# Performance work log

Measured on AMD Instinct MI355X. Metric: run time of the kernel, lower is better.

Reference implementation:

```python
import jax, jax.numpy as jnp
import numpy as np

D = 40       # d_model
SL = 10      # sequenceLength
AN = 268     # actionNum
B = 8192     # batch


def relu6(x):
    return jnp.clip(x, 0.0, 6.0)


def setup_inputs() -> dict:
    key = jax.random.key(0)
    ks = jax.random.split(key, 16)
    s = 1.0 / np.sqrt(D)
    X = jax.random.randint(ks[0], (B, SL, 4), 0, AN)
    t1 = jax.random.randint(ks[1], (B, SL - 1), 0, 7)
    t2 = jax.random.randint(ks[2], (B, SL - 1), 0, 8)
    # per-step Linear(1, D): weight [D,1] -> store as [SL-1, D]; kaiming-uniform bound 1/sqrt(1)=1
    Ew = jax.random.uniform(ks[3], (SL - 1, D), minval=-1.0, maxval=1.0)
    Eb = jax.random.uniform(ks[4], (SL - 1, D), minval=-1.0, maxval=1.0)
    Qw = jax.random.uniform(ks[5], (SL - 1, D, D), minval=-s, maxval=s)
    Qb = jax.random.uniform(ks[6], (SL - 1, D), minval=-s, maxval=s)
    Lw = jax.random.uniform(ks[7], (SL - 1, D * D, D), minval=-s, maxval=s)
    Lb = jax.random.uniform(ks[8], (SL - 1, D * D), minval=-s, maxval=s)
    Mw = jax.random.uniform(ks[9], (SL - 1, D, D), minval=-s, maxval=s)
    Mb = jax.random.uniform(ks[10], (SL - 1, D), minval=-s, maxval=s)
    Tw = jax.random.uniform(ks[11], (AN, D), minval=-s, maxval=s)
    Tb = jax.random.uniform(ks[12], (AN,), minval=-s, maxval=s)
    emb = jax.random.normal(ks[13], (AN, D))
    return dict(X=X, t1=t1, t2=t2, Ew=Ew, Eb=Eb, Qw=Qw, Qb=Qb, Lw=Lw, Lb=Lb,
                Mw=Mw, Mb=Mb, Tw=Tw, Tb=Tb, emb=emb)


def reference(X, t1, t2, Ew, Eb, Qw, Qb, Lw, Lb, Mw, Mb, Tw, Tb, emb):
    b = X.shape[0]
    t = (t1 * 8 + t2).astype(jnp.float32)          # [B, SL-1]
    ae = emb[X[:, :SL - 1, 3]]                     # [B, SL-1, D]

    def step(carry, xs):
        h0, p0 = carry
        ew, eb, qw, qb, lw, lb, mw, mb, ti, ei = xs
        # E(t_i) + Q(p0), both [B, D]
        p1 = relu6(ti[:, None] * ew[None, :] + eb + p0 @ qw.T + qb)
        # hypernetwork-generated per-sample matrix [B, D, D]
        jt = relu6(p1 @ lw.T + lb).reshape(b, D, D)
        tt = jnp.einsum('bd,bde->be', h0, jt)
        h1 = relu6(ei @ mw.T + mb + tt)
        return (h1, p1), None

    xs = (Ew, Eb, Qw, Qb, Lw, Lb, Mw, Mb, t.T, jnp.swapaxes(ae, 0, 1))
    init = (jnp.zeros((b, D), jnp.float32), jnp.zeros((b, D), jnp.float32))
    (h0, _), _ = jax.lax.scan(step, init, xs)
    return h0 @ Tw.T + Tb                          # [B, AN]
```

## Files before the change

### kernel.cpp

```cpp
#include <hip/hip_runtime.h>

#define DD 40
#define SLM1 9
#define ANUM 268
#define MB 32

typedef __attribute__((ext_vector_type(8))) short short8;
typedef __attribute__((ext_vector_type(4))) float f32x4;
typedef __attribute__((ext_vector_type(16))) float f32x16;

#define WS_LW ((size_t)0)
#define WS_QW ((size_t)1105920)
#define WS_MW ((size_t)1133568)
#define WS_TW ((size_t)1161216)

__device__ __forceinline__ unsigned short f2bf(float f){
  unsigned int u = __float_as_uint(f);
  u += 0x7FFFu + ((u >> 16) & 1u);
  return (unsigned short)(u >> 16);
}
__device__ __forceinline__ float relu6f(float v){
  return fminf(fmaxf(v, 0.0f), 6.0f);
}

__device__ __forceinline__ f32x16 mfma3(short8 a0, short8 a1, short8 a2,
                                        short8 b0, short8 b1, short8 b2){
  f32x16 c = {0,0,0,0,0,0,0,0,0,0,0,0,0,0,0,0};
  c = __builtin_amdgcn_mfma_f32_32x32x16_bf16(a0, b0, c, 0, 0, 0);
  c = __builtin_amdgcn_mfma_f32_32x32x16_bf16(a1, b1, c, 0, 0, 0);
  c = __builtin_amdgcn_mfma_f32_32x32x16_bf16(a2, b2, c, 0, 0, 0);
  return c;
}

__global__ __launch_bounds__(256)
void prep_frags(const float* __restrict__ Qw, const float* __restrict__ Lw,
                const float* __restrict__ Mw, const float* __restrict__ Tw,
                const float* __restrict__ Ew, const float* __restrict__ Eb,
                const float* __restrict__ Qb, const float* __restrict__ Lb,
                const float* __restrict__ Mb, const float* __restrict__ Tb,
                unsigned short* __restrict__ ws)
{
  const int bid = blockIdx.x, tid = threadIdx.x;
  if (bid < 360){
    int s = bid / 40, d = bid - s*40;
    unsigned short* dst = ws + WS_LW + (size_t)bid*3072;
    const float* W = Lw + (size_t)s*64000;
    const float* bv = Lb + (size_t)s*1600;
    for (int i = tid; i < 3072; i += 256){
      int et = i / 1536, r = i - et*1536;
      int kf = r >> 9, q = r & 511, l = q >> 3, j = q & 7;
      int k = kf*16 + ((l >> 5) << 3) + j;
      int e = et*32 + (l & 31);
      float v = 0.f;
      if (e < DD){
        int n = d*DD + e;
        if (k < DD) v = W[n*DD + k];
        else if (k == DD) v = bv[n];
      }
      dst[i] = f2bf(v);
    }
  } else if (bid < 369){
    int s = bid - 360;
    unsigned short* dst = ws + WS_QW + (size_t)s*3072;
    const float* W = Qw + (size_t)s*1600;
    for (int i = tid; i < 3072; i += 256){
      int et = i / 1536, r = i - et*1536;
      int kf = r >> 9, q = r & 511, l = q >> 3, j = q & 7;
      int k = kf*16 + ((l >> 5) << 3) + j;
      int jc = et*32 + (l & 31);
      float v = 0.f;
      if (jc < DD){
        if (k < DD) v = W[jc*DD + k];
        else if (k == DD) v = Eb[s*DD + jc] + Qb[s*DD + jc];
        else if (k == DD+1) v = Ew[s*DD + jc];
      }
      dst[i] = f2bf(v);
    }
  } else if (bid < 378){
    int s = bid - 369;
    unsigned short* dst = ws + WS_MW + (size_t)s*3072;
    const float* W = Mw + (size_t)s*1600;
    for (int i = tid; i < 3072; i += 256){
      int et = i / 1536, r = i - et*1536;
      int kf = r >> 9, q = r & 511, l = q >> 3, j = q & 7;
      int k = kf*16 + ((l >> 5) << 3) + j;
      int e = et*32 + (l & 31);
      float v = 0.f;
      if (e < DD){
        if (k < DD) v = W[e*DD + k];
        else if (k == DD) v = Mb[s*DD + e];
      }
      dst[i] = f2bf(v);
    }
  } else {
    int t = bid - 378;
    unsigned short* dst = ws + WS_TW + (size_t)t*1536;
    for (int i = tid; i < 1536; i += 256){
      int kf = i >> 9, q = i & 511, l = q >> 3, j = q & 7;
      int k = kf*16 + ((l >> 5) << 3) + j;
      int a = t*32 + (l & 31);
      float v = 0.f;
      if (a < ANUM){
        if (k < DD) v = Tw[(size_t)a*DD + k];
        else if (k == DD) v = Tb[a];
      }
      dst[i] = f2bf(v);
    }
  }
}

__global__ __launch_bounds__(512)
void star_main(const int* __restrict__ X,
               const int* __restrict__ T1,
               const int* __restrict__ T2,
               const float* __restrict__ emb,
               const unsigned short* __restrict__ ws,
               float* __restrict__ out)
{
  __shared__ __align__(16) unsigned short pbuf[2][3072];
  __shared__ __align__(16) unsigned short aebf[2][3072];
  __shared__ __align__(16) float hT[2][DD*36];
  __shared__ __align__(16) float red[8][MB*DD];
  __shared__ int   aeidx[SLM1][MB];
  __shared__ float tvtab[SLM1][MB];

  const int tid = threadIdx.x;
  const int w = __builtin_amdgcn_readfirstlane(tid >> 6);
  const int l = tid & 63;
  const int col = l & 31, half = l >> 5;
  const int row0 = blockIdx.x * MB;

  {
    unsigned int* p = (unsigned int*)&pbuf[0][0];
    for (int i = tid; i < 3072; i += 512) p[i] = 0u;
    unsigned int* a = (unsigned int*)&aebf[0][0];
    for (int i = tid; i < 3072; i += 512) a[i] = 0u;
    float* rr = &red[0][0];
    for (int i = tid; i < 8*MB*DD; i += 512) rr[i] = 0.f;
  }
  if (tid < MB*SLM1){
    int m = tid / SLM1, s = tid - m*SLM1;
    int r = row0 + m;
    aeidx[s][m] = X[(size_t)r*40 + s*4 + 3];
    tvtab[s][m] = (float)(T1[r*SLM1 + s]*8 + T2[r*SLM1 + s]);
  }
  __syncthreads();
  if (tid < MB){
    int off = 2*1024 + (tid + 32)*8;
    pbuf[0][off] = 0x3F80; pbuf[1][off] = 0x3F80;
    aebf[0][off] = 0x3F80; aebf[1][off] = 0x3F80;
    pbuf[0][off+1] = f2bf(tvtab[0][tid]);
    pbuf[1][off+1] = f2bf(tvtab[1][tid]);
  }
  if (tid < 320){
    int m = tid / 10, q4 = tid - m*10;
    float4 v4 = *(const float4*)(emb + (size_t)aeidx[0][m]*DD + q4*4);
    #pragma unroll
    for (int c2 = 0; c2 < 4; ++c2){
      int k = q4*4 + c2, kf = k >> 4, kk = k & 15;
      aebf[0][kf*1024 + (m + ((kk >> 3) << 5))*8 + (kk & 7)] = f2bf(((const float*)&v4)[c2]);
    }
  }
  __syncthreads();
  if (w < 2){
    short8 a0 = ((const short8*)&pbuf[0][0])[l];
    short8 a1 = ((const short8*)&pbuf[0][1024])[l];
    short8 a2 = ((const short8*)&pbuf[0][2048])[l];
    const unsigned short* qwb = ws + WS_QW + w*1536;
    f32x16 c = mfma3(a0, a1, a2, ((const short8*)qwb)[l],
                     ((const short8*)(qwb+512))[l], ((const short8*)(qwb+1024))[l]);
    int j = w*32 + col;
    if (j < DD){
      int kf = j >> 4, kk = j & 15;
      #pragma unroll
      for (int r = 0; r < 16; ++r){
        int m = (r & 3) + ((r >> 2) << 3) + (half << 2);
        pbuf[1][kf*1024 + (m + ((kk >> 3) << 5))*8 + (kk & 7)] = f2bf(relu6f(c[r]));
      }
    }
  }
  __syncthreads();

  for (int s = 0; s < SLM1; ++s){
    const int pcur = (s + 1) & 1;
    const int hrd  = s & 1;

    float4 gv; int gm = 0, gq = 0;
    const bool dog = (s < 8) && (tid < 320);
    if (dog){
      gm = tid / 10; gq = tid - gm*10;
      gv = *(const float4*)(emb + (size_t)aeidx[s+1][gm]*DD + gq*4);
    }
    if (s > 0){
      short8 pa0 = ((const short8*)&pbuf[pcur][0])[l];
      short8 pa1 = ((const short8*)&pbuf[pcur][1024])[l];
      short8 pa2 = ((const short8*)&pbuf[pcur][2048])[l];
      const unsigned short* lwb = ws + WS_LW + (size_t)(s*40)*3072;
      const float* hbase = &hT[hrd][half << 2];

      f32x16 tt0 = {0,0,0,0,0,0,0,0,0,0,0,0,0,0,0,0};
      {
        const unsigned short* fb = lwb + (size_t)w*3072;
        short8 cb0 = ((const short8*)fb)[l];
        short8 cb1 = ((const short8*)(fb + 512))[l];
        short8 cb2 = ((const short8*)(fb + 1024))[l];
        #pragma unroll
        for (int i = 0; i < 5; ++i){
          short8 nb0, nb1, nb2;
          if (i < 4){
            const unsigned short* nf = lwb + (size_t)((i+1)*8 + w)*3072;
            nb0 = ((const short8*)nf)[l];
            nb1 = ((const short8*)(nf + 512))[l];
            nb2 = ((const short8*)(nf + 1024))[l];
          }
          f32x16 c = mfma3(pa0, pa1, pa2, cb0, cb1, cb2);
          const float* hb = hbase + (i*8 + w)*36;
          #pragma unroll
          for (int g = 0; g < 4; ++g){
            f32x4 hg = *(const f32x4*)(hb + g*8);
            #pragma unroll
            for (int q = 0; q < 4; ++q)
              tt0[g*4+q] = fmaf(hg[q], relu6f(c[g*4+q]), tt0[g*4+q]);
          }
          if (i < 4){ cb0 = nb0; cb1 = nb1; cb2 = nb2; }
        }
      }
      #pragma unroll
      for (int r = 0; r < 16; ++r){
        int m = (r & 3) + ((r >> 2) << 3) + (half << 2);
        red[w][m*DD + col] = tt0[r];
      }

      f32x16 tt1 = {0,0,0,0,0,0,0,0,0,0,0,0,0,0,0,0};
      {
        short8 cb0 = {0,0,0,0,0,0,0,0}, cb1 = {0,0,0,0,0,0,0,0}, cb2 = {0,0,0,0,0,0,0,0};
        if (col < 8){
          const unsigned short* fb = lwb + (size_t)w*3072 + 1536;
          cb0 = ((const short8*)fb)[l];
          cb1 = ((const short8*)(fb + 512))[l];
          cb2 = ((const short8*)(fb + 1024))[l];
        }
        #pragma unroll
        for (int i = 0; i < 5; ++i){
          short8 nb0 = {0,0,0,0,0,0,0,0}, nb1 = {0,0,0,0,0,0,0,0}, nb2 = {0,0,0,0,0,0,0,0};
          if (i < 4 && col < 8){
            const unsigned short* nf = lwb + (size_t)((i+1)*8 + w)*3072 + 1536;
            nb0 = ((const short8*)nf)[l];
            nb1 = ((const short8*)(nf + 512))[l];
            nb2 = ((const short8*)(nf + 1024))[l];
          }
          f32x16 c = mfma3(pa0, pa1, pa2, cb0, cb1, cb2);
          const float* hb = hbase + (i*8 + w)*36;
          #pragma unroll
          for (int g = 0; g < 4; ++g){
            f32x4 hg = *(const f32x4*)(hb + g*8);
            #pragma unroll
            for (int q = 0; q < 4; ++q)
              tt1[g*4+q] = fmaf(hg[q], relu6f(c[g*4+q]), tt1[g*4+q]);
          }
          if (i < 4){ cb0 = nb0; cb1 = nb1; cb2 = nb2; }
        }
      }
      if (col < 8){
        #pragma unroll
        for (int r = 0; r < 16; ++r){
          int m = (r & 3) + ((r >> 2) << 3) + (half << 2);
          red[w][m*DD + 32 + col] = tt1[r];
        }
      }
    }
    if (dog){
      unsigned short* dst = &aebf[(s+1) & 1][0];
      #pragma unroll
      for (int c2 = 0; c2 < 4; ++c2){
        int k = gq*4 + c2, kf = k >> 4, kk = k & 15;
        dst[kf*1024 + (gm + ((kk >> 3) << 5))*8 + (kk & 7)] = f2bf(((const float*)&gv)[c2]);
      }
    }
    if (s <= 6 && tid < MB)
      pbuf[s & 1][2*1024 + (tid + 32)*8 + 1] = f2bf(tvtab[s+2][tid]);
    __syncthreads();

    if (w < 2){
      short8 a0 = ((const short8*)&aebf[s & 1][0])[l];
      short8 a1 = ((const short8*)&aebf[s & 1][1024])[l];
      short8 a2 = ((const short8*)&aebf[s & 1][2048])[l];
      const unsigned short* mwb = ws + WS_MW + (size_t)s*3072 + w*1536;
      int e = w*32 + col;
      f32x16 c = {0,0,0,0,0,0,0,0,0,0,0,0,0,0,0,0};
      if (e < DD){
        #pragma unroll
        for (int r = 0; r < 16; ++r){
          int m = (r & 3) + ((r >> 2) << 3) + (half << 2);
          float acc = red[0][m*DD + e];
          #pragma unroll
          for (int dp = 1; dp < 8; ++dp) acc += red[dp][m*DD + e];
          c[r] = acc;
        }
      }
      c = __builtin_amdgcn_mfma_f32_32x32x16_bf16(a0, ((const short8*)mwb)[l], c, 0, 0, 0);
      c = __builtin_amdgcn_mfma_f32_32x32x16_bf16(a1, ((const short8*)(mwb+512))[l], c, 0, 0, 0);
      c = __builtin_amdgcn_mfma_f32_32x32x16_bf16(a2, ((const short8*)(mwb+1024))[l], c, 0, 0, 0);
      if (e < DD){
        int kf = e >> 4, kk = e & 15;
        #pragma unroll
        for (int r = 0; r < 16; ++r){
          int m = (r & 3) + ((r >> 2) << 3) + (half << 2);
          float v = relu6f(c[r]);
          hT[(s+1) & 1][e*36 + m] = v;
          if (s == SLM1-1)
            aebf[1][kf*1024 + (m + ((kk >> 3) << 5))*8 + (kk & 7)] = f2bf(v);
        }
      }
    } else if (w < 4 && s < 8){
      const int et = w - 2;
      short8 a0 = ((const short8*)&pbuf[pcur][0])[l];
      short8 a1 = ((const short8*)&pbuf[pcur][1024])[l];
      short8 a2 = ((const short8*)&pbuf[pcur][2048])[l];
      const unsigned short* qwb = ws + WS_QW + (size_t)(s+1)*3072 + et*1536;
      f32x16 c = mfma3(a0, a1, a2, ((const short8*)qwb)[l],
                       ((const short8*)(qwb+512))[l], ((const short8*)(qwb+1024))[l]);
      int j = et*32 + col;
      if (j < DD){
        int kf = j >> 4, kk = j & 15;
        #pragma unroll
        for (int r = 0; r < 16; ++r){
          int m = (r & 3) + ((r >> 2) << 3) + (half << 2);
          pbuf[s & 1][kf*1024 + (m + ((kk >> 3) << 5))*8 + (kk & 7)] = f2bf(relu6f(c[r]));
        }
      }
    }
    __syncthreads();
  }

  for (int t = w; t < 9; t += 8){
    short8 a0 = ((const short8*)&aebf[1][0])[l];
    short8 a1 = ((const short8*)&aebf[1][1024])[l];
    short8 a2 = ((const short8*)&aebf[1][2048])[l];
    const unsigned short* twb = ws + WS_TW + (size_t)t*1536;
    f32x16 c = mfma3(a0, a1, a2, ((const short8*)twb)[l],
                     ((const short8*)(twb+512))[l], ((const short8*)(twb+1024))[l]);
    int a = t*32 + col;
    if (a < ANUM){
      #pragma unroll
      for (int r = 0; r < 16; ++r){
        int m = (r & 3) + ((r >> 2) << 3) + (half << 2);
        out[(size_t)(row0 + m)*ANUM + a] = c[r];
      }
    }
  }
}

extern "C" void kernel_launch(void* const* d_in, const int* in_sizes, int n_in,
                              void* d_out, int out_size, void* d_ws, size_t ws_size,
                              hipStream_t stream) {
  const int*   X  = (const int*)  d_in[0];
  const int*   T1 = (const int*)  d_in[1];
  const int*   T2 = (const int*)  d_in[2];
  const float* Ew = (const float*)d_in[3];
  const float* Eb = (const float*)d_in[4];
  const float* Qw = (const float*)d_in[5];
  const float* Qb = (const float*)d_in[6];
  const float* Lw = (const float*)d_in[7];
  const float* Lb = (const float*)d_in[8];
  const float* Mw = (const float*)d_in[9];
  const float* Mb = (const float*)d_in[10];
  const float* Tw = (const float*)d_in[11];
  const float* Tb = (const float*)d_in[12];
  const float* em = (const float*)d_in[13];
  unsigned short* ws = (unsigned short*)d_ws;
  float* out = (float*)d_out;

  prep_frags<<<dim3(387), dim3(256), 0, stream>>>(Qw, Lw, Mw, Tw, Ew, Eb, Qb,
                                                  Lb, Mb, Tb, ws);
  star_main<<<dim3(8192 / MB), dim3(512), 0, stream>>>(X, T1, T2, em, ws, out);
}
```

Before: 59.62 us.

## Repack hypernetwork tail columns densely and reduce via LDS atomics

```diff
diff --git a/kernel.cpp b/kernel.cpp
--- a/kernel.cpp
+++ b/kernel.cpp
@@ -4,15 +4,17 @@
 #define SLM1 9
 #define ANUM 268
 #define MB 32
+#define RSZ 2560
 
 typedef __attribute__((ext_vector_type(8))) short short8;
 typedef __attribute__((ext_vector_type(4))) float f32x4;
 typedef __attribute__((ext_vector_type(16))) float f32x16;
 
-#define WS_LW ((size_t)0)
-#define WS_QW ((size_t)1105920)
-#define WS_MW ((size_t)1133568)
-#define WS_TW ((size_t)1161216)
+#define WS_LWF ((size_t)0)
+#define WS_LWT ((size_t)552960)
+#define WS_QW  ((size_t)691200)
+#define WS_MW  ((size_t)718848)
+#define WS_TW  ((size_t)746496)
 
 __device__ __forceinline__ unsigned short f2bf(float f){
   unsigned int u = __float_as_uint(f);
@@ -43,24 +45,39 @@
   const int bid = blockIdx.x, tid = threadIdx.x;
   if (bid < 360){
     int s = bid / 40, d = bid - s*40;
-    unsigned short* dst = ws + WS_LW + (size_t)bid*3072;
+    unsigned short* dst = ws + WS_LWF + (size_t)bid*1536;
     const float* W = Lw + (size_t)s*64000;
     const float* bv = Lb + (size_t)s*1600;
-    for (int i = tid; i < 3072; i += 256){
-      int et = i / 1536, r = i - et*1536;
-      int kf = r >> 9, q = r & 511, l = q >> 3, j = q & 7;
-      int k = kf*16 + ((l >> 5) << 3) + j;
-      int e = et*32 + (l & 31);
-      float v = 0.f;
-      if (e < DD){
-        int n = d*DD + e;
-        if (k < DD) v = W[n*DD + k];
-        else if (k == DD) v = bv[n];
-      }
-      dst[i] = f2bf(v);
-    }
-  } else if (bid < 369){
-    int s = bid - 360;
+    for (int i = tid; i < 1536; i += 256){
+      int kf = i >> 9, q = i & 511, l = q >> 3, j = q & 7;
+      int k = kf*16 + ((l >> 5) << 3) + j;
+      int e = l & 31;
+      int n = d*DD + e;
+      float v = 0.f;
+      if (k < DD) v = W[n*DD + k];
+      else if (k == DD) v = bv[n];
+      dst[i] = f2bf(v);
+    }
+  } else if (bid < 450){
+    int t = bid - 360;
+    int s = t / 10, tt = t - s*10;
+    unsigned short* dst = ws + WS_LWT + (size_t)t*1536;
+    const float* W = Lw + (size_t)s*64000;
+    const float* bv = Lb + (size_t)s*1600;
+    for (int i = tid; i < 1536; i += 256){
+      int kf = i >> 9, q = i & 511, l = q >> 3, j = q & 7;
+      int k = kf*16 + ((l >> 5) << 3) + j;
+      int c = l & 31;
+      int d = 4*tt + (c >> 3);
+      int e = 32 + (c & 7);
+      int n = d*DD + e;
+      float v = 0.f;
+      if (k < DD) v = W[n*DD + k];
+      else if (k == DD) v = bv[n];
+      dst[i] = f2bf(v);
+    }
+  } else if (bid < 459){
+    int s = bid - 450;
     unsigned short* dst = ws + WS_QW + (size_t)s*3072;
     const float* W = Qw + (size_t)s*1600;
     for (int i = tid; i < 3072; i += 256){
@@ -76,8 +93,8 @@
       }
       dst[i] = f2bf(v);
     }
-  } else if (bid < 378){
-    int s = bid - 369;
+  } else if (bid < 468){
+    int s = bid - 459;
     unsigned short* dst = ws + WS_MW + (size_t)s*3072;
     const float* W = Mw + (size_t)s*1600;
     for (int i = tid; i < 3072; i += 256){
@@ -93,7 +110,7 @@
       dst[i] = f2bf(v);
     }
   } else {
-    int t = bid - 378;
+    int t = bid - 468;
     unsigned short* dst = ws + WS_TW + (size_t)t*1536;
     for (int i = tid; i < 1536; i += 256){
       int kf = i >> 9, q = i & 511, l = q >> 3, j = q & 7;
@@ -120,7 +137,7 @@
   __shared__ __align__(16) unsigned short pbuf[2][3072];
   __shared__ __align__(16) unsigned short aebf[2][3072];
   __shared__ __align__(16) float hT[2][DD*36];
-  __shared__ __align__(16) float red[8][MB*DD];
+  __shared__ __align__(16) float red[2][RSZ];
   __shared__ int   aeidx[SLM1][MB];
   __shared__ float tvtab[SLM1][MB];
 
@@ -135,8 +152,10 @@
     for (int i = tid; i < 3072; i += 512) p[i] = 0u;
     unsigned int* a = (unsigned int*)&aebf[0][0];
     for (int i = tid; i < 3072; i += 512) a[i] = 0u;
+    float* ht = &hT[0][0];
+    for (int i = tid; i < 2*DD*36; i += 512) ht[i] = 0.f;
     float* rr = &red[0][0];
-    for (int i = tid; i < 8*MB*DD; i += 512) rr[i] = 0.f;
+    for (int i = tid; i < 2*RSZ; i += 512) rr[i] = 0.f;
   }
   if (tid < MB*SLM1){
     int m = tid / SLM1, s = tid - m*SLM1;
@@ -195,78 +214,73 @@
       short8 pa0 = ((const short8*)&pbuf[pcur][0])[l];
       short8 pa1 = ((const short8*)&pbuf[pcur][1024])[l];
       short8 pa2 = ((const short8*)&pbuf[pcur][2048])[l];
-      const unsigned short* lwb = ws + WS_LW + (size_t)(s*40)*3072;
       const float* hbase = &hT[hrd][half << 2];
-
-      f32x16 tt0 = {0,0,0,0,0,0,0,0,0,0,0,0,0,0,0,0};
+      float* rd = &red[s & 1][0];
+
+      f32x16 tt = {0,0,0,0,0,0,0,0,0,0,0,0,0,0,0,0};
       {
-        const unsigned short* fb = lwb + (size_t)w*3072;
-        short8 cb0 = ((const short8*)fb)[l];
-        short8 cb1 = ((const short8*)(fb + 512))[l];
-        short8 cb2 = ((const short8*)(fb + 1024))[l];
+        const unsigned short* lwf = ws + WS_LWF + (size_t)(s*40)*1536;
+        const unsigned short* f0 = lwf + (size_t)w*1536;
+        short8 b00 = ((const short8*)f0)[l];
+        short8 b01 = ((const short8*)(f0 + 512))[l];
+        short8 b02 = ((const short8*)(f0 + 1024))[l];
+        const unsigned short* f1 = lwf + (size_t)(8 + w)*1536;
+        short8 b10 = ((const short8*)f1)[l];
+        short8 b11 = ((const short8*)(f1 + 512))[l];
+        short8 b12 = ((const short8*)(f1 + 1024))[l];
         #pragma unroll
         for (int i = 0; i < 5; ++i){
           short8 nb0, nb1, nb2;
-          if (i < 4){
-            const unsigned short* nf = lwb + (size_t)((i+1)*8 + w)*3072;
+          if (i < 3){
+            const unsigned short* nf = lwf + (size_t)((i+2)*8 + w)*1536;
             nb0 = ((const short8*)nf)[l];
             nb1 = ((const short8*)(nf + 512))[l];
             nb2 = ((const short8*)(nf + 1024))[l];
           }
-          f32x16 c = mfma3(pa0, pa1, pa2, cb0, cb1, cb2);
+          f32x16 c = mfma3(pa0, pa1, pa2, b00, b01, b02);
           const float* hb = hbase + (i*8 + w)*36;
           #pragma unroll
           for (int g = 0; g < 4; ++g){
             f32x4 hg = *(const f32x4*)(hb + g*8);
             #pragma unroll
             for (int q = 0; q < 4; ++q)
-              tt0[g*4+q] = fmaf(hg[q], relu6f(c[g*4+q]), tt0[g*4+q]);
+              tt[g*4+q] = fmaf(hg[q], relu6f(c[g*4+q]), tt[g*4+q]);
           }
-          if (i < 4){ cb0 = nb0; cb1 = nb1; cb2 = nb2; }
-        }
-      }
+          b00 = b10; b01 = b11; b02 = b12;
+          if (i < 3){ b10 = nb0; b11 = nb1; b12 = nb2; }
+        }
+      }
+      const unsigned short* lwt = ws + WS_LWT + (size_t)(s*10)*1536;
+      const unsigned short* ft = lwt + (size_t)w*1536;
+      short8 t0 = ((const short8*)ft)[l];
+      short8 t1 = ((const short8*)(ft + 512))[l];
+      short8 t2 = ((const short8*)(ft + 1024))[l];
       #pragma unroll
       for (int r = 0; r < 16; ++r){
         int m = (r & 3) + ((r >> 2) << 3) + (half << 2);
-        red[w][m*DD + col] = tt0[r];
-      }
-
-      f32x16 tt1 = {0,0,0,0,0,0,0,0,0,0,0,0,0,0,0,0};
-      {
-        short8 cb0 = {0,0,0,0,0,0,0,0}, cb1 = {0,0,0,0,0,0,0,0}, cb2 = {0,0,0,0,0,0,0,0};
-        if (col < 8){
-          const unsigned short* fb = lwb + (size_t)w*3072 + 1536;
-          cb0 = ((const short8*)fb)[l];
-          cb1 = ((const short8*)(fb + 512))[l];
-          cb2 = ((const short8*)(fb + 1024))[l];
-        }
+        atomicAdd(&rd[m*DD + col], tt[r]);
+      }
+      int tti = w;
+      while (true){
+        f32x16 c = mfma3(pa0, pa1, pa2, t0, t1, t2);
+        int dt = 4*tti + (col >> 3);
+        int e2 = 32 + (col & 7);
+        const float* hb = &hT[hrd][dt*36 + (half << 2)];
         #pragma unroll
-        for (int i = 0; i < 5; ++i){
-          short8 nb0 = {0,0,0,0,0,0,0,0}, nb1 = {0,0,0,0,0,0,0,0}, nb2 = {0,0,0,0,0,0,0,0};
-          if (i < 4 && col < 8){
-            const unsigned short* nf = lwb + (size_t)((i+1)*8 + w)*3072 + 1536;
-            nb0 = ((const short8*)nf)[l];
-            nb1 = ((const short8*)(nf + 512))[l];
-            nb2 = ((const short8*)(nf + 1024))[l];
+        for (int g = 0; g < 4; ++g){
+          f32x4 hg = *(const f32x4*)(hb + g*8);
+          #pragma unroll
+          for (int q = 0; q < 4; ++q){
+            int m = q + (g << 3) + (half << 2);
+            atomicAdd(&rd[m*DD + e2], hg[q]*relu6f(c[g*4+q]));
           }
-          f32x16 c = mfma3(pa0, pa1, pa2, cb0, cb1, cb2);
-          const float* hb = hbase + (i*8 + w)*36;
-          #pragma unroll
-          for (int g = 0; g < 4; ++g){
-            f32x4 hg = *(const f32x4*)(hb + g*8);
-            #pragma unroll
-            for (int q = 0; q < 4; ++q)
-              tt1[g*4+q] = fmaf(hg[q], relu6f(c[g*4+q]), tt1[g*4+q]);
-          }
-          if (i < 4){ cb0 = nb0; cb1 = nb1; cb2 = nb2; }
-        }
-      }
-      if (col < 8){
-        #pragma unroll
-        for (int r = 0; r < 16; ++r){
-          int m = (r & 3) + ((r >> 2) << 3) + (half << 2);
-          red[w][m*DD + 32 + col] = tt1[r];
-        }
+        }
+        tti += 8;
+        if (tti >= 10) break;
+        const unsigned short* f2p = lwt + (size_t)tti*1536;
+        t0 = ((const short8*)f2p)[l];
+        t1 = ((const short8*)(f2p + 512))[l];
+        t2 = ((const short8*)(f2p + 1024))[l];
       }
     }
     if (dog){
@@ -292,10 +306,7 @@
         #pragma unroll
         for (int r = 0; r < 16; ++r){
           int m = (r & 3) + ((r >> 2) << 3) + (half << 2);
-          float acc = red[0][m*DD + e];
-          #pragma unroll
-          for (int dp = 1; dp < 8; ++dp) acc += red[dp][m*DD + e];
-          c[r] = acc;
+          c[r] = red[s & 1][m*DD + e];
         }
       }
       c = __builtin_amdgcn_mfma_f32_32x32x16_bf16(a0, ((const short8*)mwb)[l], c, 0, 0, 0);
@@ -312,23 +323,28 @@
             aebf[1][kf*1024 + (m + ((kk >> 3) << 5))*8 + (kk & 7)] = f2bf(v);
         }
       }
-    } else if (w < 4 && s < 8){
-      const int et = w - 2;
-      short8 a0 = ((const short8*)&pbuf[pcur][0])[l];
-      short8 a1 = ((const short8*)&pbuf[pcur][1024])[l];
-      short8 a2 = ((const short8*)&pbuf[pcur][2048])[l];
-      const unsigned short* qwb = ws + WS_QW + (size_t)(s+1)*3072 + et*1536;
-      f32x16 c = mfma3(a0, a1, a2, ((const short8*)qwb)[l],
-                       ((const short8*)(qwb+512))[l], ((const short8*)(qwb+1024))[l]);
-      int j = et*32 + col;
-      if (j < DD){
-        int kf = j >> 4, kk = j & 15;
-        #pragma unroll
-        for (int r = 0; r < 16; ++r){
-          int m = (r & 3) + ((r >> 2) << 3) + (half << 2);
-          pbuf[s & 1][kf*1024 + (m + ((kk >> 3) << 5))*8 + (kk & 7)] = f2bf(relu6f(c[r]));
-        }
-      }
+    } else if (w < 4){
+      if (s < 8){
+        const int et = w - 2;
+        short8 a0 = ((const short8*)&pbuf[pcur][0])[l];
+        short8 a1 = ((const short8*)&pbuf[pcur][1024])[l];
+        short8 a2 = ((const short8*)&pbuf[pcur][2048])[l];
+        const unsigned short* qwb = ws + WS_QW + (size_t)(s+1)*3072 + et*1536;
+        f32x16 c = mfma3(a0, a1, a2, ((const short8*)qwb)[l],
+                         ((const short8*)(qwb+512))[l], ((const short8*)(qwb+1024))[l]);
+        int j = et*32 + col;
+        if (j < DD){
+          int kf = j >> 4, kk = j & 15;
+          #pragma unroll
+          for (int r = 0; r < 16; ++r){
+            int m = (r & 3) + ((r >> 2) << 3) + (half << 2);
+            pbuf[s & 1][kf*1024 + (m + ((kk >> 3) << 5))*8 + (kk & 7)] = f2bf(relu6f(c[r]));
+          }
+        }
+      }
+    } else {
+      float* rz = &red[(s+1) & 1][0];
+      for (int i = tid - 256; i < MB*DD; i += 256) rz[i] = 0.f;
     }
     __syncthreads();
   }
@@ -371,7 +387,7 @@
   unsigned short* ws = (unsigned short*)d_ws;
   float* out = (float*)d_out;
 
-  prep_frags<<<dim3(387), dim3(256), 0, stream>>>(Qw, Lw, Mw, Tw, Ew, Eb, Qb,
+  prep_frags<<<dim3(477), dim3(256), 0, stream>>>(Qw, Lw, Mw, Tw, Ew, Eb, Qb,
                                                   Lb, Mb, Tb, ws);
   star_main<<<dim3(8192 / MB), dim3(512), 0, stream>>>(X, T1, T2, em, ws, out);
 }
```

After: 225.2 us. 278% more time.
